# Kernel optimization log

Measured on AMD Instinct MI355X. Metric: run time of the kernel, lower is better.

Reference implementation:

```python
import jax, jax.numpy as jnp
import numpy as np
import math

D_MODEL = 256
D_STATE = 16
D_CONV = 4
EXPAND = 2
N_HEADS = 4
D_INNER = EXPAND * D_MODEL          # 512
DT_RANK = (D_MODEL + 15) // 16      # 16
B_SZ, SEQ = 4, 2048


def setup_inputs() -> dict:
    key = jax.random.key(0)
    ks = jax.random.split(key, 12)
    rn = lambda i, shp, sc=0.02: jax.random.normal(ks[i], shp, dtype=jnp.float32) * sc
    x = jax.random.normal(ks[0], (B_SZ, SEQ, D_MODEL), dtype=jnp.float32)
    return dict(
        x=x,
        ln_g=jnp.ones((D_MODEL,), jnp.float32),
        ln_b=jnp.zeros((D_MODEL,), jnp.float32),
        W_in=rn(1, (D_MODEL, 2 * D_INNER)),
        conv_w=rn(2, (D_INNER, D_CONV), 0.1),
        conv_b=jnp.zeros((D_INNER,), jnp.float32),
        W_xproj=rn(3, (D_INNER, DT_RANK + 2 * D_STATE)),
        W_dt=rn(4, (DT_RANK, D_INNER), 0.1),
        b_dt=jnp.full((D_INNER,), -4.6, jnp.float32),  # softplus ~ 0.01 init
        A_log=jnp.log(jnp.tile(jnp.arange(1, D_STATE + 1, dtype=jnp.float32), (D_INNER, 1))),
        Dp=jnp.ones((D_INNER,), jnp.float32),
        W_out_m=rn(5, (D_INNER, D_MODEL)),
        W_qkv=rn(6, (D_MODEL, 3 * D_MODEL)),
        b_qkv=jnp.zeros((3 * D_MODEL,), jnp.float32),
        W_o=rn(7, (D_MODEL, D_MODEL)),
        b_o=jnp.zeros((D_MODEL,), jnp.float32),
        W_gate=rn(8, (2 * D_MODEL, D_MODEL)),
        b_gate=jnp.zeros((D_MODEL,), jnp.float32),
    )


def _sssd_forward(x, ln_g, ln_b, W_in, conv_w, conv_b, W_xproj, W_dt, b_dt,
                  A_log, Dp, W_out_m, W_qkv, b_qkv, W_o, b_o, W_gate, b_gate):
    B, L, D = x.shape
    # LayerNorm
    mu = x.mean(-1, keepdims=True)
    var = x.var(-1, keepdims=True)
    xn = (x - mu) * jax.lax.rsqrt(var + 1e-5) * ln_g + ln_b

    # ---- Mamba branch ----
    xz = xn @ W_in                      # (B,L,2*D_INNER)
    xm, z = jnp.split(xz, 2, axis=-1)
    # causal depthwise conv1d (kernel D_CONV)
    xp = jnp.pad(xm, ((0, 0), (D_CONV - 1, 0), (0, 0)))
    xc = conv_b + sum(xp[:, k:k + L, :] * conv_w[:, k] for k in range(D_CONV))
    xc = jax.nn.silu(xc)
    dbl = xc @ W_xproj                  # (B,L,DT_RANK+2*D_STATE)
    dt_in = dbl[..., :DT_RANK]
    Bm = dbl[..., DT_RANK:DT_RANK + D_STATE]
    Cm = dbl[..., DT_RANK + D_STATE:]
    dt = jax.nn.softplus(dt_in @ W_dt + b_dt)   # (B,L,D_INNER)
    A = -jnp.exp(A_log)                 # (D_INNER, D_STATE)

    def step(h, inp):
        x_t, dt_t, B_t, C_t = inp       # (B,Din),(B,Din),(B,N),(B,N)
        dA = jnp.exp(dt_t[..., None] * A)               # (B,Din,N)
        h = dA * h + (dt_t * x_t)[..., None] * B_t[:, None, :]
        y = jnp.einsum('bdn,bn->bd', h, C_t)
        return h, y

    h0 = jnp.zeros((B, D_INNER, D_STATE), x.dtype)
    xs = (jnp.swapaxes(xc, 0, 1), jnp.swapaxes(dt, 0, 1),
          jnp.swapaxes(Bm, 0, 1), jnp.swapaxes(Cm, 0, 1))
    _, ys = jax.lax.scan(step, h0, xs)
    y = jnp.swapaxes(ys, 0, 1) + xc * Dp
    y = y * jax.nn.silu(z)
    ssm_out = y @ W_out_m               # (B,L,D)

    # ---- MHSA branch (eval: no dropout) ----
    hd = D // N_HEADS
    qkv = xn @ W_qkv + b_qkv
    q, k, v = jnp.split(qkv, 3, axis=-1)
    sh = lambda t: t.reshape(B, L, N_HEADS, hd).transpose(0, 2, 1, 3)
    q, k, v = sh(q), sh(k), sh(v)
    scores = jnp.einsum('bhqd,bhkd->bhqk', q, k) * (1.0 / math.sqrt(hd))
    attn = jax.nn.softmax(scores, axis=-1)
    o = jnp.einsum('bhqk,bhkd->bhqd', attn, v).transpose(0, 2, 1, 3).reshape(B, L, D)
    attn_out = o @ W_o + b_o

    # ---- sigmoid gate fusion ----
    gate = jax.nn.sigmoid(jnp.concatenate([ssm_out, attn_out], axis=-1) @ W_gate + b_gate)
    fused = gate * ssm_out + (1.0 - gate) * attn_out
    return x + fused


def reference(x, ln_g, ln_b, W_in, conv_w, conv_b, W_xproj, W_dt, b_dt,
              A_log, Dp, W_out_m, W_qkv, b_qkv, W_o, b_o, W_gate, b_gate):
    return _sssd_forward(x, ln_g, ln_b, W_in, conv_w, conv_b, W_xproj, W_dt, b_dt,
                         A_log, Dp, W_out_m, W_qkv, b_qkv, W_o, b_o, W_gate, b_gate)
```

## Files before the change

kernel.cpp:

```cpp
#include <hip/hip_runtime.h>
#include <math.h>

#define B_SZ 4
#define SEQ 2048
#define DM 256
#define DI 512
#define DS 16
#define DTR 16
#define NH 4
#define HD 64
#define T_TOK (B_SZ*SEQ)
#define NCH 64
#define CL (SEQ/NCH)
#define NSP 8
#define QSCALE 0.18033688f

typedef short bf16x8 __attribute__((ext_vector_type(8)));
typedef float f32x4  __attribute__((ext_vector_type(4)));
typedef float f32x16 __attribute__((ext_vector_type(16)));
typedef unsigned short u16;

__device__ __forceinline__ float sigmoidf_(float x){ return 1.f/(1.f+__expf(-x)); }
__device__ __forceinline__ u16 f2bf(float x){
  unsigned int u = __float_as_uint(x);
  u += 0x7fffu + ((u>>16)&1u);
  return (u16)(u>>16);
}
__device__ __forceinline__ float bf2f(u16 u){ return __uint_as_float(((unsigned)u)<<16); }
__device__ __forceinline__ unsigned cvt_pk_bf16(float lo, float hi){
  unsigned r;
  asm("v_cvt_pk_bf16_f32 %0, %1, %2" : "=v"(r) : "v"(lo), "v"(hi));
  return r;
}
__device__ __forceinline__ void permswap(unsigned &a, unsigned &b){
  asm volatile("v_permlane32_swap_b32 %0, %1" : "+v"(a), "+v"(b));
}
__device__ __forceinline__ float xor32f(float v){
  unsigned a = __float_as_uint(v), b = a;
  permswap(a, b);
  return __uint_as_float(a);
}

struct TcvtArgs {
  const float* src[6];
  u16* dst[6];
  int K[6];
  int Nvalid[6];
  int Npad[6];
};
__global__ __launch_bounds__(256) void tcvt_all(TcvtArgs a) {
  int wi = blockIdx.z;
  int K = a.K[wi], Nv = a.Nvalid[wi], Np = a.Npad[wi];
  int k0 = blockIdx.x*64, n0 = blockIdx.y*64;
  if (k0 >= K || n0 >= Np) return;
  __shared__ u16 tile[64][65];
  const float* src = a.src[wi];
  u16* dst = a.dst[wi];
  int tn = threadIdx.x & 63, tq = threadIdx.x >> 6;
#pragma unroll
  for (int j=0;j<16;++j){
    int kk = j*4 + tq;
    int n = n0 + tn;
    tile[tn][kk] = (n < Nv) ? f2bf(src[(size_t)(k0+kk)*Nv + n]) : (u16)0;
  }
  __syncthreads();
#pragma unroll
  for (int j=0;j<16;++j){
    int nn = j*4 + tq;
    dst[(size_t)(n0+nn)*K + k0 + tn] = tile[nn][tn];
  }
}

__global__ __launch_bounds__(256) void ln_kernel(const float* __restrict__ x,
    const float* __restrict__ g, const float* __restrict__ b,
    u16* __restrict__ xn_bf) {
  int wid = threadIdx.x >> 6;
  int lane = threadIdx.x & 63;
  int token = blockIdx.x*4 + wid;
  const float* xr = x + (size_t)token*DM;
  float4 v = *(const float4*)&xr[lane*4];
  float s  = v.x+v.y+v.z+v.w;
  float ss = v.x*v.x+v.y*v.y+v.z*v.z+v.w*v.w;
  for (int m=1;m<64;m<<=1){ s += __shfl_xor(s,m); ss += __shfl_xor(ss,m); }
  float mu  = s * (1.f/DM);
  float var = ss*(1.f/DM) - mu*mu;
  float rs  = rsqrtf(var + 1e-5f);
  float4 gv = *(const float4*)&g[lane*4];
  float4 bv = *(const float4*)&b[lane*4];
  uint2 o;
  o.x = cvt_pk_bf16((v.x-mu)*rs*gv.x + bv.x, (v.y-mu)*rs*gv.y + bv.y);
  o.y = cvt_pk_bf16((v.z-mu)*rs*gv.z + bv.z, (v.w-mu)*rs*gv.w + bv.w);
  *(uint2*)&xn_bf[(size_t)token*DM + lane*4] = o;
}

template<int ACT>
__global__ __launch_bounds__(256) void gemm_mfma(const u16* __restrict__ A,
    const u16* __restrict__ Wt, const float* __restrict__ bias,
    float* __restrict__ C, u16* __restrict__ Cbf, int K, int ldc, int nvalid,
    int qcols, float qscale, const float* __restrict__ xres,
    const float* __restrict__ cat2, u16* __restrict__ vTout,
    u16* __restrict__ qkvout,
    const u16* __restrict__ A2, const u16* __restrict__ Wt2, int K2,
    const float* __restrict__ bias2) {
  __shared__ u16 lds[12288];
  int tid = threadIdx.x;
  int m0 = blockIdx.y*128;
  int n0 = blockIdx.x*64;
  const u16* Ap = A; const u16* Wp = Wt; int Kp = K; const float* bp = bias;
  int halfsel = 0;
  if (ACT==6){
    halfsel = (blockIdx.x >= 4);
    if (halfsel){ Ap = A2; Wp = Wt2; Kp = K2; bp = bias2; }
    n0 = (blockIdx.x & 3)*64;
  }
  int w = tid>>6, l = tid&63, lq = l&15, lg = l>>4;
  int wm = w>>1, wn = w&1;
  f32x4 acc[4][2] = {};
  for (int k0 = 0; k0 < Kp; k0 += 64) {
#pragma unroll
    for (int i=0;i<4;++i){
      int gid = i*256 + tid;
      int row = gid>>3, g = gid&7;
      *(bf16x8*)&lds[row*64 + ((g ^ (row&7))*8)] =
          *(const bf16x8*)&Ap[(size_t)(m0+row)*Kp + k0 + g*8];
    }
#pragma unroll
    for (int i=0;i<2;++i){
      int gid = i*256 + tid;
      int row = gid>>3, g = gid&7;
      *(bf16x8*)&lds[8192 + row*64 + ((g ^ (row&7))*8)] =
          *(const bf16x8*)&Wp[(size_t)(n0+row)*Kp + k0 + g*8];
    }
    __syncthreads();
#pragma unroll
    for (int ks=0;ks<2;++ks){
      bf16x8 af[4], bfv[2];
#pragma unroll
      for (int mi=0;mi<4;++mi){
        int row = wm*64 + mi*16 + lq;
        af[mi] = *(bf16x8*)&lds[row*64 + (((ks*4+lg) ^ (row&7))*8)];
      }
#pragma unroll
      for (int nj=0;nj<2;++nj){
        int row = wn*32 + nj*16 + lq;
        bfv[nj] = *(bf16x8*)&lds[8192 + row*64 + (((ks*4+lg) ^ (row&7))*8)];
      }
#pragma unroll
      for (int mi=0;mi<4;++mi)
#pragma unroll
        for (int nj=0;nj<2;++nj)
          acc[mi][nj] = __builtin_amdgcn_mfma_f32_16x16x32_bf16(af[mi], bfv[nj], acc[mi][nj], 0,0,0);
    }
    __syncthreads();
  }
#pragma unroll
  for (int mi=0;mi<4;++mi){
#pragma unroll
    for (int nj=0;nj<2;++nj){
#pragma unroll
      for (int r=0;r<4;++r){
        int row = m0 + wm*64 + mi*16 + lg*4 + r;
        int col = n0 + wn*32 + nj*16 + lq;
        if (col < nvalid) {
          float v = acc[mi][nj][r];
          if (ACT==0 && bias) v += bias[col];
          if (col < qcols) v *= qscale;
          if (ACT==2) {
            if (bias) v += bias[col];
            float g = sigmoidf_(v);
            float sv = cat2[(size_t)row*512 + col];
            float av = cat2[(size_t)row*512 + 256 + col];
            C[(size_t)row*256 + col] = xres[(size_t)row*256 + col] + g*sv + (1.f-g)*av;
          } else if (ACT==5) {
            if (col < 1024) {
              Cbf[(size_t)row*1024 + col] = f2bf(v);
            } else {
              int c2 = col - 1024;
              v += bias[c2];
              if (c2 < 256) v *= qscale;
              qkvout[(size_t)row*768 + c2] = f2bf(v);
              if (c2 >= 512) {
                int bb = row>>11, ll = row&2047;
                int hh = (c2-512)>>6, dd = (c2-512)&63;
                vTout[(((size_t)(bb*4+hh))*64 + dd)*SEQ + ll] = f2bf(v);
              }
            }
          } else if (ACT==6) {
            if (bp) v += bp[col];
            C[(size_t)row*512 + halfsel*256 + col] = v;
            Cbf[(size_t)row*512 + halfsel*256 + col] = f2bf(v);
          } else {
            if (C)   C[(size_t)row*ldc + col] = v;
            if (Cbf) Cbf[(size_t)row*ldc + col] = f2bf(v);
          }
        }
      }
    }
  }
}

__global__ __launch_bounds__(256) void conv_kernel(const u16* __restrict__ xzb,
    const float* __restrict__ cw, const float* __restrict__ cb,
    u16* __restrict__ xc_bf) {
  int idx = blockIdx.x*256 + threadIdx.x;
  int d2 = (idx & 255)*2;
  int t = idx >> 8;
  int l = t & (SEQ-1);
  float acc0 = cb[d2], acc1 = cb[d2+1];
  float4 wA = *(const float4*)&cw[d2*4];
  float4 wB = *(const float4*)&cw[d2*4+4];
  const u16* base = xzb + (size_t)t*1024 + d2;
  ushort2 v;
  if (l>=3){ v = *(const ushort2*)&base[-3*1024]; acc0 += bf2f(v.x)*wA.x; acc1 += bf2f(v.y)*wB.x; }
  if (l>=2){ v = *(const ushort2*)&base[-2*1024]; acc0 += bf2f(v.x)*wA.y; acc1 += bf2f(v.y)*wB.y; }
  if (l>=1){ v = *(const ushort2*)&base[-1*1024]; acc0 += bf2f(v.x)*wA.z; acc1 += bf2f(v.y)*wB.z; }
  v = *(const ushort2*)&base[0];
  acc0 += bf2f(v.x)*wA.w; acc1 += bf2f(v.y)*wB.w;
  float r0 = acc0 * sigmoidf_(acc0);
  float r1 = acc1 * sigmoidf_(acc1);
  *(unsigned*)&xc_bf[(size_t)t*DI + d2] = cvt_pk_bf16(r0, r1);
}

__global__ __launch_bounds__(256) void dt_kernel(const float* __restrict__ dbl,
    const float* __restrict__ Wdt, const float* __restrict__ bdt,
    u16* __restrict__ dt) {
  __shared__ float sdbl[4][16];
  int wid = threadIdx.x>>6, lane = threadIdx.x&63;
  int token = blockIdx.x*4 + wid;
  if (lane < 16) sdbl[wid][lane] = dbl[(size_t)token*48 + lane];
  __syncthreads();
  float din[16];
#pragma unroll
  for (int k=0;k<16;++k) din[k] = sdbl[wid][k];
#pragma unroll
  for (int r=0;r<8;++r){
    int d = lane + r*64;
    float acc = bdt[d];
#pragma unroll
    for (int k=0;k<16;++k) acc += din[k]*Wdt[k*DI+d];
    float sp = (acc > 20.f) ? acc : log1pf(__expf(acc));
    dt[(size_t)token*DI+d] = f2bf(sp);
  }
}

__global__ __launch_bounds__(512) void scan_p1(const u16* __restrict__ xc_bf,
    const u16* __restrict__ dt, const float* __restrict__ dbl,
    const float* __restrict__ A_log, u16* __restrict__ Pws, u16* __restrict__ Hws) {
  __shared__ float sB[CL][16];
  int d = threadIdx.x;
  int bc = blockIdx.x;
  int b = bc >> 6, c = bc & 63;
  {
    int t = threadIdx.x >> 4, n = threadIdx.x & 15;
    sB[t][n] = dbl[((size_t)b*SEQ + c*CL + t)*48 + DTR + n];
  }
  __syncthreads();
  float An[16];
#pragma unroll
  for (int i=0;i<4;++i){
    float4 a = *(const float4*)&A_log[d*16 + i*4];
    An[i*4+0] = -__expf(a.x); An[i*4+1] = -__expf(a.y);
    An[i*4+2] = -__expf(a.z); An[i*4+3] = -__expf(a.w);
  }
  float h[16] = {};
  float P[16];
#pragma unroll
  for (int n=0;n<16;++n) P[n] = 1.f;
  size_t tok = (size_t)b*SEQ + c*CL;
  for (int t=0;t<CL;++t,++tok){
    float dtv = bf2f(dt[tok*DI+d]);
    float xcv = bf2f(xc_bf[tok*DI+d]);
    float u = dtv*xcv;
    float4 B0 = *(float4*)&sB[t][0];
    float4 B1 = *(float4*)&sB[t][4];
    float4 B2 = *(float4*)&sB[t][8];
    float4 B3 = *(float4*)&sB[t][12];
    float Bv[16] = {B0.x,B0.y,B0.z,B0.w,B1.x,B1.y,B1.z,B1.w,
                    B2.x,B2.y,B2.z,B2.w,B3.x,B3.y,B3.z,B3.w};
#pragma unroll
    for (int n=0;n<16;++n){
      float e = __expf(dtv*An[n]);
      P[n] *= e;
      h[n] = e*h[n] + u*Bv[n];
    }
  }
  size_t base = (((size_t)b*NCH + c)*DI + d)*16;
#pragma unroll
  for (int i=0;i<8;++i){
    *(unsigned*)&Pws[base + i*2] = cvt_pk_bf16(P[i*2], P[i*2+1]);
    *(unsigned*)&Hws[base + i*2] = cvt_pk_bf16(h[i*2], h[i*2+1]);
  }
}

__global__ __launch_bounds__(256) void scan_combine(const u16* __restrict__ Pws,
    const u16* __restrict__ Hws, u16* __restrict__ H0ws) {
  int gid = blockIdx.x*256 + threadIdx.x;
  int b  = gid >> 13;
  int dn = gid & 8191;
  float h0 = 0.f;
#pragma unroll 4
  for (int c=0;c<NCH;++c){
    size_t idx = ((size_t)(b*NCH+c)<<13) + dn;
    H0ws[idx] = f2bf(h0);
    h0 = bf2f(Pws[idx])*h0 + bf2f(Hws[idx]);
  }
}

__global__ __launch_bounds__(512) void scan_p2(const u16* __restrict__ xc_bf,
    const u16* __restrict__ dt, const float* __restrict__ dbl,
    const float* __restrict__ A_log, const float* __restrict__ Dp,
    const u16* __restrict__ xzb, const u16* __restrict__ H0ws,
    u16* __restrict__ ygate_bf) {
  __shared__ float sBC[CL][32];
  int d = threadIdx.x;
  int bc = blockIdx.x;
  int b = bc >> 6, c = bc & 63;
#pragma unroll
  for (int i=0;i<2;++i){
    int idx = i*512 + threadIdx.x;
    int t = idx >> 5, q = idx & 31;
    sBC[t][q] = dbl[((size_t)b*SEQ + c*CL + t)*48 + DTR + q];
  }
  __syncthreads();
  float An[16];
#pragma unroll
  for (int i=0;i<4;++i){
    float4 a = *(const float4*)&A_log[d*16 + i*4];
    An[i*4+0] = -__expf(a.x); An[i*4+1] = -__expf(a.y);
    An[i*4+2] = -__expf(a.z); An[i*4+3] = -__expf(a.w);
  }
  float Dd = Dp[d];
  float h[16];
  size_t base = (((size_t)b*NCH + c)*DI + d)*16;
  {
    bf16x8 h8a = *(const bf16x8*)&H0ws[base];
    bf16x8 h8b = *(const bf16x8*)&H0ws[base+8];
#pragma unroll
    for (int n=0;n<8;++n){ h[n] = bf2f((u16)h8a[n]); h[8+n] = bf2f((u16)h8b[n]); }
  }
  size_t tok = (size_t)b*SEQ + c*CL;
  for (int t=0;t<CL;++t,++tok){
    float dtv = bf2f(dt[tok*DI+d]);
    float xcv = bf2f(xc_bf[tok*DI+d]);
    float zv  = bf2f(xzb[tok*1024 + DI + d]);
    float u = dtv*xcv;
    float4 B0 = *(float4*)&sBC[t][0];
    float4 B1 = *(float4*)&sBC[t][4];
    float4 B2 = *(float4*)&sBC[t][8];
    float4 B3 = *(float4*)&sBC[t][12];
    float4 C0 = *(float4*)&sBC[t][16];
    float4 C1 = *(float4*)&sBC[t][20];
    float4 C2 = *(float4*)&sBC[t][24];
    float4 C3 = *(float4*)&sBC[t][28];
    float Bv[16] = {B0.x,B0.y,B0.z,B0.w,B1.x,B1.y,B1.z,B1.w,
                    B2.x,B2.y,B2.z,B2.w,B3.x,B3.y,B3.z,B3.w};
    float Cv[16] = {C0.x,C0.y,C0.z,C0.w,C1.x,C1.y,C1.z,C1.w,
                    C2.x,C2.y,C2.z,C2.w,C3.x,C3.y,C3.z,C3.w};
    float y = 0.f;
#pragma unroll
    for (int n=0;n<16;++n){
      float e = __expf(dtv*An[n]);
      h[n] = e*h[n] + u*Bv[n];
      y += h[n]*Cv[n];
    }
    y += xcv*Dd;
    ygate_bf[tok*DI + d] = f2bf(y * (zv*sigmoidf_(zv)));
  }
}

__global__ __launch_bounds__(256) void attn_mfma_kernel(const u16* __restrict__ qkvb,
    const u16* __restrict__ vT,
    u16* __restrict__ Opart, float* __restrict__ ml) {
  __shared__ u16 lds[8192];
  int H = blockIdx.x + 8*blockIdx.y + 128*(int)blockIdx.z;
  int cx = H & 7, kk = H >> 3;
  int xq = kk & 7;
  int G  = cx*16 + (kk >> 3);
  int bh = G & 15, s = G >> 4;
  int b = bh>>2, h = bh&3;
  int tid = threadIdx.x;
  int w = tid>>6, l = tid&63;
  int lo32 = l & 31;
  int hi = l >> 5;
  size_t bbase = (size_t)b*SEQ;
  size_t vbase = (size_t)bh*HD*SEQ;
  int q_base = xq*256 + w*64;

  bf16x8 qf[2][4];
#pragma unroll
  for (int qg=0; qg<2; ++qg)
#pragma unroll
    for (int dsl=0; dsl<4; ++dsl)
      qf[qg][dsl] = *(const bf16x8*)&qkvb[(bbase + q_base + qg*32 + lo32)*768 + h*HD + dsl*16 + hi*8];

  float m_[2] = {-1e30f,-1e30f}, l_[2] = {0.f,0.f};
  f32x16 oacc[2][2] = {};

  int srow = tid>>3, sg = tid&7;
  int kt0 = s*4;
  bf16x8 kreg[2], vreg[2];

#define LOADT(kt) { \
  kreg[0] = *(const bf16x8*)&qkvb[(bbase + (size_t)(kt)*64 + srow)*768 + 256 + h*HD + sg*8]; \
  kreg[1] = *(const bf16x8*)&qkvb[(bbase + (size_t)(kt)*64 + srow + 32)*768 + 256 + h*HD + sg*8]; \
  vreg[0] = *(const bf16x8*)&vT[vbase + (size_t)srow*SEQ + (kt)*64 + sg*8]; \
  vreg[1] = *(const bf16x8*)&vT[vbase + (size_t)(srow+32)*SEQ + (kt)*64 + sg*8]; }
#define STORET() { \
  *(bf16x8*)&lds[srow*64 + ((sg ^ (srow&7))*8)] = kreg[0]; \
  *(bf16x8*)&lds[(srow+32)*64 + ((sg ^ ((srow+32)&7))*8)] = kreg[1]; \
  *(bf16x8*)&lds[4096 + srow*64 + ((sg ^ (srow&7))*8)] = vreg[0]; \
  *(bf16x8*)&lds[4096 + (srow+32)*64 + ((sg ^ ((srow+32)&7))*8)] = vreg[1]; }
#define EXCH(X, Y, s_own, s_oth) { \
  unsigned xa = (X), yb = (Y); \
  permswap(xa, yb); \
  s_own = (l < 32) ? (X) : xa; \
  s_oth = (l < 32) ? yb : (Y); }

  LOADT(kt0);
  for (int it=0; it<4; ++it){
    __syncthreads();
    STORET();
    __syncthreads();
    if (it < 3) LOADT(kt0+it+1);

#pragma unroll
    for (int t32=0; t32<2; ++t32){
      int krow = t32*32 + lo32;
      bf16x8 kf[4];
#pragma unroll
      for (int dsl=0; dsl<4; ++dsl)
        kf[dsl] = *(bf16x8*)&lds[krow*64 + (((dsl*2 + hi) ^ (krow&7))*8)];

      bf16x8 pf[2][2];
#pragma unroll
      for (int qg=0; qg<2; ++qg){
        f32x16 sacc = {0,0,0,0,0,0,0,0,0,0,0,0,0,0,0,0};
#pragma unroll
        for (int dsl=0; dsl<4; ++dsl)
          sacc = __builtin_amdgcn_mfma_f32_32x32x16_bf16(kf[dsl], qf[qg][dsl], sacc, 0,0,0);

        float tm = sacc[0];
#pragma unroll
        for (int r=1;r<16;++r) tm = fmaxf(tm, sacc[r]);
        tm = fmaxf(tm, xor32f(tm));
        if (__any(tm - m_[qg] > 8.f)) {
          float mn = fmaxf(m_[qg], tm);
          float sc = exp2f(m_[qg] - mn);
          m_[qg] = mn;
          l_[qg] *= sc;
#pragma unroll
          for (int r=0;r<16;++r){ oacc[qg][0][r] *= sc; oacc[qg][1][r] *= sc; }
        }
        float p[16];
        float ps = 0.f;
#pragma unroll
        for (int r=0;r<16;++r){ p[r] = exp2f(sacc[r] - m_[qg]); ps += p[r]; }
        ps += xor32f(ps);
        l_[qg] += ps;

        unsigned A0 = cvt_pk_bf16(p[0],p[1]),  A1 = cvt_pk_bf16(p[2],p[3]);
        unsigned B0 = cvt_pk_bf16(p[4],p[5]),  B1 = cvt_pk_bf16(p[6],p[7]);
        unsigned C0 = cvt_pk_bf16(p[8],p[9]),  C1 = cvt_pk_bf16(p[10],p[11]);
        unsigned D0 = cvt_pk_bf16(p[12],p[13]),D1 = cvt_pk_bf16(p[14],p[15]);
        unsigned s0,s1,s2,s3,s4,s5,s6,s7;
        EXCH(A0,B0,s0,s2); EXCH(A1,B1,s1,s3);
        EXCH(C0,D0,s4,s6); EXCH(C1,D1,s5,s7);
        ((unsigned*)&pf[qg][0])[0]=s0; ((unsigned*)&pf[qg][0])[1]=s1;
        ((unsigned*)&pf[qg][0])[2]=s2; ((unsigned*)&pf[qg][0])[3]=s3;
        ((unsigned*)&pf[qg][1])[0]=s4; ((unsigned*)&pf[qg][1])[1]=s5;
        ((unsigned*)&pf[qg][1])[2]=s6; ((unsigned*)&pf[qg][1])[3]=s7;
      }

#pragma unroll
      for (int dtile=0; dtile<2; ++dtile){
        int vrow = dtile*32 + lo32;
        bf16x8 vf0 = *(bf16x8*)&lds[4096 + vrow*64 + (((t32*4 + 0 + hi) ^ (vrow&7))*8)];
        bf16x8 vf1 = *(bf16x8*)&lds[4096 + vrow*64 + (((t32*4 + 2 + hi) ^ (vrow&7))*8)];
        oacc[0][dtile] = __builtin_amdgcn_mfma_f32_32x32x16_bf16(vf0, pf[0][0], oacc[0][dtile], 0,0,0);
        oacc[0][dtile] = __builtin_amdgcn_mfma_f32_32x32x16_bf16(vf1, pf[0][1], oacc[0][dtile], 0,0,0);
        oacc[1][dtile] = __builtin_amdgcn_mfma_f32_32x32x16_bf16(vf0, pf[1][0], oacc[1][dtile], 0,0,0);
        oacc[1][dtile] = __builtin_amdgcn_mfma_f32_32x32x16_bf16(vf1, pf[1][1], oacc[1][dtile], 0,0,0);
      }
    }
  }
#undef LOADT
#undef STORET
#undef EXCH

  int sidx = bh*NSP + s;
#pragma unroll
  for (int qg=0; qg<2; ++qg){
    size_t rb = ((size_t)sidx*SEQ + q_base + qg*32 + lo32)*64;
#pragma unroll
    for (int dtile=0; dtile<2; ++dtile){
#pragma unroll
      for (int rg=0; rg<4; ++rg){
        uint2 pk;
        pk.x = cvt_pk_bf16(oacc[qg][dtile][rg*4+0], oacc[qg][dtile][rg*4+1]);
        pk.y = cvt_pk_bf16(oacc[qg][dtile][rg*4+2], oacc[qg][dtile][rg*4+3]);
        *(uint2*)&Opart[rb + dtile*32 + rg*8 + 4*hi] = pk;
      }
    }
    if (l < 32){
      ml[((size_t)sidx*SEQ + q_base + qg*32 + lo32)*2    ] = m_[qg];
      ml[((size_t)sidx*SEQ + q_base + qg*32 + lo32)*2 + 1] = l_[qg];
    }
  }
}

__global__ __launch_bounds__(256) void attn_merge_kernel(const u16* __restrict__ Opart,
    const float* __restrict__ ml, u16* __restrict__ attn_bf) {
  int w = threadIdx.x>>6, lane = threadIdx.x&63;
  int R = blockIdx.x*4 + w;
  int bh = R>>11, q = R&2047;
  float m[NSP], lv[NSP];
#pragma unroll
  for (int s=0;s<NSP;++s){
    m[s]  = ml[((size_t)(bh*NSP+s)*SEQ + q)*2];
    lv[s] = ml[((size_t)(bh*NSP+s)*SEQ + q)*2 + 1];
  }
  float ms = m[0];
#pragma unroll
  for (int s=1;s<NSP;++s) ms = fmaxf(ms, m[s]);
  float o = 0.f, lsum = 0.f;
#pragma unroll
  for (int s=0;s<NSP;++s){
    float wsc = exp2f(m[s]-ms);
    lsum += wsc*lv[s];
    o += wsc*bf2f(Opart[((size_t)(bh*NSP+s)*SEQ + q)*64 + lane]);
  }
  size_t token = (size_t)(bh>>2)*SEQ + q;
  attn_bf[token*DM + (bh&3)*HD + lane] = f2bf(o/lsum);
}

extern "C" void kernel_launch(void* const* d_in, const int* in_sizes, int n_in,
                              void* d_out, int out_size, void* d_ws, size_t ws_size,
                              hipStream_t stream) {
  const float* x      = (const float*)d_in[0];
  const float* ln_g   = (const float*)d_in[1];
  const float* ln_b   = (const float*)d_in[2];
  const float* W_in   = (const float*)d_in[3];
  const float* conv_w = (const float*)d_in[4];
  const float* conv_b = (const float*)d_in[5];
  const float* W_xproj= (const float*)d_in[6];
  const float* W_dt   = (const float*)d_in[7];
  const float* b_dt   = (const float*)d_in[8];
  const float* A_log  = (const float*)d_in[9];
  const float* Dp     = (const float*)d_in[10];
  const float* W_out_m= (const float*)d_in[11];
  const float* W_qkv  = (const float*)d_in[12];
  const float* b_qkv  = (const float*)d_in[13];
  const float* W_o    = (const float*)d_in[14];
  const float* b_o    = (const float*)d_in[15];
  const float* W_gate = (const float*)d_in[16];
  const float* b_gate = (const float*)d_in[17];
  float* out = (float*)d_out;

  float* ws = (float*)d_ws;
  u16*   xn_bf   = (u16*)(ws);
  u16*   xzb     = (u16*)(ws + 1048576);
  u16*   qkv_bf  = (u16*)(ws + 9437184);
  u16*   xc_bf   = (u16*)(ws + 12582912);
  float* dblb    = ws + 16777216;
  u16*   dtb     = (u16*)(ws + 17170432);
  u16*   ygate_bf= (u16*)(ws + 21364736);
  u16*   attn_bf = (u16*)(ws + 23461888);
  float* catb    = ws + 24510464;
  u16*   catb_bf = (u16*)(ws + 28704768);
  float* gateb   = ws + 30801920;
  u16*   Wt_all  = (u16*)(ws + 32899072);
  u16*   Opart = (u16*)(ws + 1048576);
  float* mlb   = (float*)xn_bf;
  u16*   vTb   = (u16*)gateb;
  u16*   Pws   = (u16*)catb;
  u16*   Hws   = (u16*)(catb + 1048576);
  u16*   H0ws  = (u16*)(catb + 2097152);

  u16* Wt_in   = Wt_all;
  u16* Wt_qkv  = Wt_all + 262144;
  u16* Wt_out  = Wt_all + 458752;
  u16* Wt_o    = Wt_all + 589824;
  u16* Wt_gate = Wt_all + 655360;
  u16* Wt_xp   = Wt_all + 786432;

  TcvtArgs ta;
  ta.src[0]=W_in;    ta.dst[0]=Wt_in;   ta.K[0]=256; ta.Nvalid[0]=1024; ta.Npad[0]=1024;
  ta.src[1]=W_qkv;   ta.dst[1]=Wt_qkv;  ta.K[1]=256; ta.Nvalid[1]=768;  ta.Npad[1]=768;
  ta.src[2]=W_out_m; ta.dst[2]=Wt_out;  ta.K[2]=512; ta.Nvalid[2]=256;  ta.Npad[2]=256;
  ta.src[3]=W_o;     ta.dst[3]=Wt_o;    ta.K[3]=256; ta.Nvalid[3]=256;  ta.Npad[3]=256;
  ta.src[4]=W_gate;  ta.dst[4]=Wt_gate; ta.K[4]=512; ta.Nvalid[4]=256;  ta.Npad[4]=256;
  ta.src[5]=W_xproj; ta.dst[5]=Wt_xp;   ta.K[5]=512; ta.Nvalid[5]=48;   ta.Npad[5]=64;
  tcvt_all<<<dim3(8,16,6), 256, 0, stream>>>(ta);

  ln_kernel<<<T_TOK/4, 256, 0, stream>>>(x, ln_g, ln_b, xn_bf);
  gemm_mfma<5><<<dim3(28,64), 256, 0, stream>>>(xn_bf, Wt_in, b_qkv, nullptr, xzb, 256, 0, 1792, 0, QSCALE, nullptr, nullptr, vTb, qkv_bf, nullptr, nullptr, 0, nullptr);
  conv_kernel<<<T_TOK, 256, 0, stream>>>(xzb, conv_w, conv_b, xc_bf);
  gemm_mfma<0><<<dim3(1,64), 256, 0, stream>>>(xc_bf, Wt_xp, nullptr, dblb, nullptr, 512, 48, 48, 0, 1.f, nullptr, nullptr, nullptr, nullptr, nullptr, nullptr, 0, nullptr);
  dt_kernel<<<T_TOK/4, 256, 0, stream>>>(dblb, W_dt, b_dt, dtb);
  scan_p1<<<B_SZ*NCH, 512, 0, stream>>>(xc_bf, dtb, dblb, A_log, Pws, Hws);
  scan_combine<<<128, 256, 0, stream>>>(Pws, Hws, H0ws);
  scan_p2<<<B_SZ*NCH, 512, 0, stream>>>(xc_bf, dtb, dblb, A_log, Dp, xzb, H0ws, ygate_bf);
  attn_mfma_kernel<<<dim3(8, 16, 8), 256, 0, stream>>>(qkv_bf, vTb, Opart, mlb);
  attn_merge_kernel<<<8192, 256, 0, stream>>>(Opart, mlb, attn_bf);
  gemm_mfma<6><<<dim3(8,64), 256, 0, stream>>>(ygate_bf, Wt_out, nullptr, catb, catb_bf, 512, 512, 256, 0, 1.f, nullptr, nullptr, nullptr, nullptr, attn_bf, Wt_o, 256, b_o);
  gemm_mfma<2><<<dim3(4,64), 256, 0, stream>>>(catb_bf, Wt_gate, b_gate, out, nullptr, 512, 256, 256, 0, 1.f, x, catb, nullptr, nullptr, nullptr, nullptr, 0, b_gate);
}
```

Before: 239.0 us.

## Load attention K/V fragments directly from global memory and halve key splits

The attention kernel no longer stages K and V tiles through shared memory with double-buffered register prefetch and barriers. Each wave now reads its K and V MFMA fragments straight from global memory (qkv buffer and transposed V). The key-split count NSP drops from 8 to 4, so each block walks 8 key tiles instead of 4, the grid is halved, and the merge kernel has fewer partials to combine. This removes the LDS traffic and the synchronisation. In exchange, the four waves of a block fetch the same K/V data separately through the caches, global load latency is no longer hidden by prefetch, and fewer blocks are available to fill the GPU.

```diff
diff --git a/kernel.cpp b/kernel.cpp
--- a/kernel.cpp
+++ b/kernel.cpp
@@ -12,7 +12,7 @@
 #define T_TOK (B_SZ*SEQ)
 #define NCH 64
 #define CL (SEQ/NCH)
-#define NSP 8
+#define NSP 4
 #define QSCALE 0.18033688f
 
 typedef short bf16x8 __attribute__((ext_vector_type(8)));
@@ -371,11 +371,10 @@
 __global__ __launch_bounds__(256) void attn_mfma_kernel(const u16* __restrict__ qkvb,
     const u16* __restrict__ vT,
     u16* __restrict__ Opart, float* __restrict__ ml) {
-  __shared__ u16 lds[8192];
   int H = blockIdx.x + 8*blockIdx.y + 128*(int)blockIdx.z;
   int cx = H & 7, kk = H >> 3;
   int xq = kk & 7;
-  int G  = cx*16 + (kk >> 3);
+  int G  = cx*8 + (kk >> 3);
   int bh = G & 15, s = G >> 4;
   int b = bh>>2, h = bh&3;
   int tid = threadIdx.x;
@@ -396,40 +395,26 @@
   float m_[2] = {-1e30f,-1e30f}, l_[2] = {0.f,0.f};
   f32x16 oacc[2][2] = {};
 
-  int srow = tid>>3, sg = tid&7;
-  int kt0 = s*4;
-  bf16x8 kreg[2], vreg[2];
-
-#define LOADT(kt) { \
-  kreg[0] = *(const bf16x8*)&qkvb[(bbase + (size_t)(kt)*64 + srow)*768 + 256 + h*HD + sg*8]; \
-  kreg[1] = *(const bf16x8*)&qkvb[(bbase + (size_t)(kt)*64 + srow + 32)*768 + 256 + h*HD + sg*8]; \
-  vreg[0] = *(const bf16x8*)&vT[vbase + (size_t)srow*SEQ + (kt)*64 + sg*8]; \
-  vreg[1] = *(const bf16x8*)&vT[vbase + (size_t)(srow+32)*SEQ + (kt)*64 + sg*8]; }
-#define STORET() { \
-  *(bf16x8*)&lds[srow*64 + ((sg ^ (srow&7))*8)] = kreg[0]; \
-  *(bf16x8*)&lds[(srow+32)*64 + ((sg ^ ((srow+32)&7))*8)] = kreg[1]; \
-  *(bf16x8*)&lds[4096 + srow*64 + ((sg ^ (srow&7))*8)] = vreg[0]; \
-  *(bf16x8*)&lds[4096 + (srow+32)*64 + ((sg ^ ((srow+32)&7))*8)] = vreg[1]; }
 #define EXCH(X, Y, s_own, s_oth) { \
   unsigned xa = (X), yb = (Y); \
   permswap(xa, yb); \
   s_own = (l < 32) ? (X) : xa; \
   s_oth = (l < 32) ? yb : (Y); }
 
-  LOADT(kt0);
-  for (int it=0; it<4; ++it){
-    __syncthreads();
-    STORET();
-    __syncthreads();
-    if (it < 3) LOADT(kt0+it+1);
-
+  for (int kt=s*8; kt<s*8+8; ++kt){
 #pragma unroll
     for (int t32=0; t32<2; ++t32){
-      int krow = t32*32 + lo32;
+      const u16* kbase = &qkvb[(bbase + (size_t)kt*64 + t32*32 + lo32)*768 + 256 + h*HD + hi*8];
       bf16x8 kf[4];
 #pragma unroll
       for (int dsl=0; dsl<4; ++dsl)
-        kf[dsl] = *(bf16x8*)&lds[krow*64 + (((dsl*2 + hi) ^ (krow&7))*8)];
+        kf[dsl] = *(const bf16x8*)&kbase[dsl*16];
+      const u16* vb0 = &vT[vbase + (size_t)(lo32     )*SEQ + kt*64 + t32*32 + hi*8];
+      const u16* vb1 = &vT[vbase + (size_t)(32 + lo32)*SEQ + kt*64 + t32*32 + hi*8];
+      bf16x8 vf00 = *(const bf16x8*)&vb0[0];
+      bf16x8 vf01 = *(const bf16x8*)&vb0[16];
+      bf16x8 vf10 = *(const bf16x8*)&vb1[0];
+      bf16x8 vf11 = *(const bf16x8*)&vb1[16];
 
       bf16x8 pf[2][2];
 #pragma unroll
@@ -471,20 +456,16 @@
         ((unsigned*)&pf[qg][1])[2]=s6; ((unsigned*)&pf[qg][1])[3]=s7;
       }
 
-#pragma unroll
-      for (int dtile=0; dtile<2; ++dtile){
-        int vrow = dtile*32 + lo32;
-        bf16x8 vf0 = *(bf16x8*)&lds[4096 + vrow*64 + (((t32*4 + 0 + hi) ^ (vrow&7))*8)];
-        bf16x8 vf1 = *(bf16x8*)&lds[4096 + vrow*64 + (((t32*4 + 2 + hi) ^ (vrow&7))*8)];
-        oacc[0][dtile] = __builtin_amdgcn_mfma_f32_32x32x16_bf16(vf0, pf[0][0], oacc[0][dtile], 0,0,0);
-        oacc[0][dtile] = __builtin_amdgcn_mfma_f32_32x32x16_bf16(vf1, pf[0][1], oacc[0][dtile], 0,0,0);
-        oacc[1][dtile] = __builtin_amdgcn_mfma_f32_32x32x16_bf16(vf0, pf[1][0], oacc[1][dtile], 0,0,0);
-        oacc[1][dtile] = __builtin_amdgcn_mfma_f32_32x32x16_bf16(vf1, pf[1][1], oacc[1][dtile], 0,0,0);
-      }
-    }
-  }
-#undef LOADT
-#undef STORET
+      oacc[0][0] = __builtin_amdgcn_mfma_f32_32x32x16_bf16(vf00, pf[0][0], oacc[0][0], 0,0,0);
+      oacc[0][0] = __builtin_amdgcn_mfma_f32_32x32x16_bf16(vf01, pf[0][1], oacc[0][0], 0,0,0);
+      oacc[0][1] = __builtin_amdgcn_mfma_f32_32x32x16_bf16(vf10, pf[0][0], oacc[0][1], 0,0,0);
+      oacc[0][1] = __builtin_amdgcn_mfma_f32_32x32x16_bf16(vf11, pf[0][1], oacc[0][1], 0,0,0);
+      oacc[1][0] = __builtin_amdgcn_mfma_f32_32x32x16_bf16(vf00, pf[1][0], oacc[1][0], 0,0,0);
+      oacc[1][0] = __builtin_amdgcn_mfma_f32_32x32x16_bf16(vf01, pf[1][1], oacc[1][0], 0,0,0);
+      oacc[1][1] = __builtin_amdgcn_mfma_f32_32x32x16_bf16(vf10, pf[1][0], oacc[1][1], 0,0,0);
+      oacc[1][1] = __builtin_amdgcn_mfma_f32_32x32x16_bf16(vf11, pf[1][1], oacc[1][1], 0,0,0);
+    }
+  }
 #undef EXCH
 
   int sidx = bh*NSP + s;
@@ -600,7 +581,7 @@
   scan_p1<<<B_SZ*NCH, 512, 0, stream>>>(xc_bf, dtb, dblb, A_log, Pws, Hws);
   scan_combine<<<128, 256, 0, stream>>>(Pws, Hws, H0ws);
   scan_p2<<<B_SZ*NCH, 512, 0, stream>>>(xc_bf, dtb, dblb, A_log, Dp, xzb, H0ws, ygate_bf);
-  attn_mfma_kernel<<<dim3(8, 16, 8), 256, 0, stream>>>(qkv_bf, vTb, Opart, mlb);
+  attn_mfma_kernel<<<dim3(8, 16, 4), 256, 0, stream>>>(qkv_bf, vTb, Opart, mlb);
   attn_merge_kernel<<<8192, 256, 0, stream>>>(Opart, mlb, attn_bf);
   gemm_mfma<6><<<dim3(8,64), 256, 0, stream>>>(ygate_bf, Wt_out, nullptr, catb, catb_bf, 512, 512, 256, 0, 1.f, nullptr, nullptr, nullptr, nullptr, attn_bf, Wt_o, 256, b_o);
   gemm_mfma<2><<<dim3(4,64), 256, 0, stream>>>(catb_bf, Wt_gate, b_gate, out, nullptr, 512, 256, 256, 0, 1.f, x, catb, nullptr, nullptr, nullptr, nullptr, 0, b_gate);
```

After: 234.8 us. Within noise of the previous version (-1.8%).
